# Kernel optimization log

Hardware: AMD Instinct MI355X
Metric: run time of the kernel (lower is better)

Reference implementation:

```python
import jax, jax.numpy as jnp
import numpy as np

EMB = 1024
HEADS = 16
B, N = 2, 2048

def setup_inputs() -> dict:
    key = jax.random.key(0)
    ks = jax.random.split(key, 9)
    s = 1.0 / np.sqrt(EMB)
    return {
        "x": jax.random.normal(ks[0], (B, N, EMB), dtype=jnp.float32),
        "Wq": jax.random.normal(ks[1], (EMB, EMB), dtype=jnp.float32) * s,
        "bq": jax.random.normal(ks[2], (EMB,), dtype=jnp.float32) * 0.01,
        "Wk": jax.random.normal(ks[3], (EMB, EMB), dtype=jnp.float32) * s,
        "bk": jax.random.normal(ks[4], (EMB,), dtype=jnp.float32) * 0.01,
        "Wv": jax.random.normal(ks[5], (EMB, EMB), dtype=jnp.float32) * s,
        "bv": jax.random.normal(ks[6], (EMB,), dtype=jnp.float32) * 0.01,
        "Wo": jax.random.normal(ks[7], (EMB, EMB), dtype=jnp.float32) * s,
        "bo": jax.random.normal(ks[8], (EMB,), dtype=jnp.float32) * 0.01,
    }

def _split_heads(t):
    b, n, e = t.shape
    return t.reshape(b, n, HEADS, e // HEADS).transpose(0, 2, 1, 3)  # b h n d

def reference(x, Wq, bq, Wk, bk, Wv, bv, Wo, bo):
    q = _split_heads(x @ Wq + bq)
    k = _split_heads(x @ Wk + bk)
    v = _split_heads(x @ Wv + bv)
    # NOTE: original scales by sqrt(emb_size), not sqrt(head_dim)
    scaling = jnp.asarray(EMB, x.dtype) ** 0.5
    energy = jnp.einsum('bhqd,bhkd->bhqk', q, k)
    att = jax.nn.softmax(energy / scaling, axis=-1)
    out = jnp.einsum('bhqk,bhkd->bhqd', att, v)
    out = out.transpose(0, 2, 1, 3).reshape(x.shape[0], x.shape[1], EMB)
    return out @ Wo + bo
```

## Files before the change

kernel.cpp:

```cpp
#include <hip/hip_runtime.h>
#include <hip/hip_bf16.h>

typedef __bf16 bf16_t;
typedef bf16_t bf16x8 __attribute__((ext_vector_type(8)));
typedef float f32x4 __attribute__((ext_vector_type(4)));
typedef float f32x16 __attribute__((ext_vector_type(16)));

#define EMB 1024
#define HEADS 16
#define BATCH 2
#define SEQ 2048
#define HD 64
#define TOKENS (BATCH * SEQ)

__device__ __forceinline__ void gld16(bf16_t* lds_dst, const bf16_t* g_src) {
    __builtin_amdgcn_global_load_lds(
        (const __attribute__((address_space(1))) unsigned int*)g_src,
        (__attribute__((address_space(3))) unsigned int*)lds_dst, 16, 0, 0);
}

__device__ __forceinline__ unsigned cvt_pk_bf16(float lo, float hi) {
    unsigned r;
    asm("v_cvt_pk_bf16_f32 %0, %1, %2" : "=v"(r) : "v"(lo), "v"(hi));
    return r;
}

__device__ __forceinline__ float exp2_fast(float x) {
#if __has_builtin(__builtin_amdgcn_exp2f)
    return __builtin_amdgcn_exp2f(x);
#else
    return __expf(x * 0.69314718056f);
#endif
}

__global__ __launch_bounds__(256) void convert_x(const float* __restrict__ x,
                                                 bf16_t* __restrict__ xb) {
    size_t i = ((size_t)blockIdx.x * 256 + threadIdx.x) * 16;
    f32x4 v0 = *(const f32x4*)&x[i];
    f32x4 v1 = *(const f32x4*)&x[i + 4];
    f32x4 v2 = *(const f32x4*)&x[i + 8];
    f32x4 v3 = *(const f32x4*)&x[i + 12];
    bf16x8 o0, o1;
#pragma unroll
    for (int j = 0; j < 4; ++j) {
        o0[j] = (bf16_t)v0[j]; o0[4 + j] = (bf16_t)v1[j];
        o1[j] = (bf16_t)v2[j]; o1[4 + j] = (bf16_t)v3[j];
    }
    *(bf16x8*)&xb[i] = o0;
    *(bf16x8*)&xb[i + 8] = o1;
}

__global__ __launch_bounds__(256) void prep_w(
    const float* __restrict__ W0, const float* __restrict__ W1,
    const float* __restrict__ W2, const float* __restrict__ W3,
    bf16_t* __restrict__ T0, bf16_t* __restrict__ T1,
    bf16_t* __restrict__ T2, bf16_t* __restrict__ T3) {
    __shared__ __align__(16) bf16_t T[64][72];
    int z = blockIdx.z;
    const float* src = (z == 0) ? W0 : (z == 1) ? W1 : (z == 2) ? W2 : W3;
    bf16_t* dst = (z == 0) ? T0 : (z == 1) ? T1 : (z == 2) ? T2 : T3;
    int k0 = blockIdx.y * 64, n0 = blockIdx.x * 64;
    int r = threadIdx.x >> 2, c4 = (threadIdx.x & 3) * 16;
    f32x4 v[4];
#pragma unroll
    for (int q = 0; q < 4; ++q)
        v[q] = *(const f32x4*)&src[(size_t)(k0 + r) * 1024 + n0 + c4 + q * 4];
#pragma unroll
    for (int j = 0; j < 16; ++j) T[c4 + j][r] = (bf16_t)v[j >> 2][j & 3];
    __syncthreads();
    bf16x8 o0 = *(const bf16x8*)&T[r][c4];
    bf16x8 o1 = *(const bf16x8*)&T[r][c4 + 8];
    *(bf16x8*)&dst[(size_t)(n0 + r) * 1024 + k0 + c4] = o0;
    *(bf16x8*)&dst[(size_t)(n0 + r) * 1024 + k0 + c4 + 8] = o1;
}

__global__ __launch_bounds__(256) void vtrans(const bf16_t* __restrict__ V,
                                              bf16_t* __restrict__ Vt) {
    __shared__ __align__(16) bf16_t T[64][72];
    int bh = blockIdx.y, n0 = blockIdx.x * 64;
    int r = threadIdx.x >> 2, c4 = (threadIdx.x & 3) * 16;
    const bf16_t* src = &V[((size_t)bh * SEQ + n0 + r) * HD + c4];
    bf16x8 v0 = *(const bf16x8*)&src[0];
    bf16x8 v1 = *(const bf16x8*)&src[8];
#pragma unroll
    for (int j = 0; j < 8; ++j) { T[c4 + j][r] = v0[j]; T[c4 + 8 + j][r] = v1[j]; }
    __syncthreads();
    bf16x8 o0 = *(const bf16x8*)&T[r][c4];
    bf16x8 o1 = *(const bf16x8*)&T[r][c4 + 8];
    bf16_t* dst = &Vt[((size_t)bh * HD + r) * SEQ + n0 + c4];
    *(bf16x8*)&dst[0] = o0;
    *(bf16x8*)&dst[8] = o1;
}

template <typename TO>
__global__ __launch_bounds__(256) void gemm128(
    const bf16_t* __restrict__ A,
    const bf16_t* __restrict__ Wt0, const bf16_t* __restrict__ Wt1, const bf16_t* __restrict__ Wt2,
    const float* __restrict__ b0, const float* __restrict__ b1, const float* __restrict__ b2,
    TO* __restrict__ o0, TO* __restrict__ o1, TO* __restrict__ o2,
    int md0, int md1, int md2, float sc0, float sc1, float sc2) {
    __shared__ __align__(16) bf16_t As[128 * 32];
    __shared__ __align__(16) bf16_t Bs[128 * 32];

    const int tid = threadIdx.x, w = tid >> 6, lane = tid & 63;
    const int quad = lane >> 4, c = lane & 15;
    const int wm = (w >> 1) * 64, wn = (w & 1) * 64;
    const int m0 = blockIdx.y * 128, n0 = blockIdx.x * 128;

    const int z = blockIdx.z;
    const bf16_t* W = (z == 0) ? Wt0 : (z == 1) ? Wt1 : Wt2;
    const float* bias = (z == 0) ? b0 : (z == 1) ? b1 : b2;
    TO* out = (z == 0) ? o0 : (z == 1) ? o1 : o2;
    const int mode = (z == 0) ? md0 : (z == 1) ? md1 : md2;
    const float scale = (z == 0) ? sc0 : (z == 1) ? sc1 : sc2;

    f32x4 acc[4][4];
#pragma unroll
    for (int i = 0; i < 4; ++i)
#pragma unroll
        for (int j = 0; j < 4; ++j) acc[i][j] = (f32x4){0.f, 0.f, 0.f, 0.f};

    const int srow = lane >> 2, schunk = lane & 3;
    const bf16_t* Ag = A + (size_t)m0 * 1024;
    const bf16_t* Bg = W + (size_t)n0 * 1024;

    for (int k0 = 0; k0 < 1024; k0 += 32) {
        __syncthreads();
#pragma unroll
        for (int s = 0; s < 2; ++s) {
            int rg = (w * 2 + s) * 16;
            gld16(&As[rg * 32], &Ag[(size_t)(rg + srow) * 1024 + k0 + schunk * 8]);
            gld16(&Bs[rg * 32], &Bg[(size_t)(rg + srow) * 1024 + k0 + schunk * 8]);
        }
        __syncthreads();

        bf16x8 af[4], bfv[4];
#pragma unroll
        for (int t = 0; t < 4; ++t)
            af[t] = *(const bf16x8*)&As[(wm + t * 16 + c) * 32 + quad * 8];
#pragma unroll
        for (int t = 0; t < 4; ++t)
            bfv[t] = *(const bf16x8*)&Bs[(wn + t * 16 + c) * 32 + quad * 8];
#pragma unroll
        for (int mt = 0; mt < 4; ++mt)
#pragma unroll
            for (int nt = 0; nt < 4; ++nt)
                acc[mt][nt] = __builtin_amdgcn_mfma_f32_16x16x32_bf16(
                    af[mt], bfv[nt], acc[mt][nt], 0, 0, 0);
    }

#pragma unroll
    for (int nt = 0; nt < 4; ++nt) {
        int col = n0 + wn + nt * 16 + c;
        float bv = bias[col];
#pragma unroll
        for (int mt = 0; mt < 4; ++mt)
#pragma unroll
            for (int r = 0; r < 4; ++r) {
                int row = m0 + wm + mt * 16 + quad * 4 + r;
                float v = (acc[mt][nt][r] + bv) * scale;
                size_t idx;
                if (mode == 0) {
                    idx = (size_t)row * 1024 + col;
                } else {
                    int bb = row >> 11, n = row & 2047;
                    int hh = col >> 6, d = col & 63;
                    idx = ((size_t)(bb * HEADS + hh) * SEQ + n) * HD + d;
                }
                out[idx] = (TO)v;
            }
    }
}

__global__ __launch_bounds__(256) void attn_kernel(
    const bf16_t* __restrict__ Q, const bf16_t* __restrict__ K,
    const bf16_t* __restrict__ Vt, bf16_t* __restrict__ O) {
    __shared__ __align__(16) bf16_t Qs[128 * 64];
    __shared__ __align__(16) bf16_t Ks[2][64 * 64];
    __shared__ __align__(16) bf16_t Vs[2][64 * 64];

    const int tid = threadIdx.x, w = tid >> 6, lane = tid & 63;
    const int hi = lane >> 5, lq = lane & 31;

    const int lin = blockIdx.x + (blockIdx.y << 4);
    const int xcd = lin & 7, slot = lin >> 3;
    const int bh = xcd + ((slot >> 4) << 3);
    const int q0 = (slot & 15) << 7;
    const int b = bh >> 4, h = bh & 15;

    const int srow8 = lane >> 3, sch = lane & 7;

    const bf16_t* Qg = Q + ((size_t)bh * SEQ + q0) * HD;
    const bf16_t* Kg0 = K + (size_t)bh * SEQ * HD;
    const bf16_t* Vg0 = Vt + (size_t)bh * HD * SEQ;

    int sl[2], sgK[2], sgV[2];
#pragma unroll
    for (int s = 0; s < 2; ++s) {
        int rg = (w * 2 + s) * 8;
        int row = rg + srow8;
        int g = sch ^ (row & 7);
        sl[s] = rg * 64;
        sgK[s] = row * 64 + g * 8;
        sgV[s] = row * SEQ + g * 8;
    }
    int rd[4];
#pragma unroll
    for (int dc = 0; dc < 4; ++dc)
        rd[dc] = lq * 64 + (((dc * 2 + hi) ^ (lq & 7)) * 8);

#pragma unroll
    for (int s = 0; s < 4; ++s) {
        int rg = (w * 4 + s) * 8;
        int row = rg + srow8;
        int g = sch ^ (row & 7);
        gld16(&Qs[rg * 64], &Qg[(size_t)row * 64 + g * 8]);
    }
#pragma unroll
    for (int s = 0; s < 2; ++s) {
        gld16(&Ks[0][sl[s]], &Kg0[sgK[s]]);
        gld16(&Vs[0][sl[s]], &Vg0[sgV[s]]);
    }
    __syncthreads();

    bf16x8 qf[4];
#pragma unroll
    for (int dc = 0; dc < 4; ++dc)
        qf[dc] = *(const bf16x8*)&Qs[w * 2048 + rd[dc]];

    f32x16 Oacc0, Oacc1;
#pragma unroll
    for (int r = 0; r < 16; ++r) { Oacc0[r] = 0.f; Oacc1[r] = 0.f; }
    float lp = 0.f;

    const bf16_t* KgN = Kg0 + 64 * HD;
    const bf16_t* VgN = Vg0 + 64;

#define ATTN_STEP(TT, CUR)                                                     \
    {                                                                          \
        if ((TT) + 1 < SEQ / 64) {                                             \
            _Pragma("unroll")                                                  \
            for (int s = 0; s < 2; ++s) {                                      \
                gld16(&Ks[(CUR) ^ 1][sl[s]], &KgN[sgK[s]]);                    \
                gld16(&Vs[(CUR) ^ 1][sl[s]], &VgN[sgV[s]]);                    \
            }                                                                  \
            KgN += 64 * HD; VgN += 64;                                         \
        }                                                                      \
        f32x16 St0, St1;                                                       \
        _Pragma("unroll")                                                      \
        for (int r = 0; r < 16; ++r) { St0[r] = 0.f; St1[r] = 0.f; }           \
        __builtin_amdgcn_s_setprio(1);                                         \
        _Pragma("unroll")                                                      \
        for (int dc = 0; dc < 4; ++dc) {                                       \
            bf16x8 k0 = *(const bf16x8*)&Ks[CUR][rd[dc]];                      \
            bf16x8 k1 = *(const bf16x8*)&Ks[CUR][rd[dc] + 2048];               \
            St0 = __builtin_amdgcn_mfma_f32_32x32x16_bf16(k0, qf[dc], St0, 0, 0, 0); \
            St1 = __builtin_amdgcn_mfma_f32_32x32x16_bf16(k1, qf[dc], St1, 0, 0, 0); \
        }                                                                      \
        __builtin_amdgcn_s_setprio(0);                                         \
        _Pragma("unroll")                                                      \
        for (int r = 0; r < 16; ++r) {                                         \
            St0[r] = exp2_fast(St0[r]); lp += St0[r];                          \
            St1[r] = exp2_fast(St1[r]); lp += St1[r];                          \
        }                                                                      \
        bf16x8 pf[4];                                                          \
        PACKFRAG(St0, 0, 0) PACKFRAG(St0, 1, 1)                                \
        PACKFRAG(St1, 0, 2) PACKFRAG(St1, 1, 3)                                \
        __builtin_amdgcn_s_setprio(1);                                         \
        _Pragma("unroll")                                                      \
        for (int f = 0; f < 4; ++f) {                                          \
            bf16x8 v0 = *(const bf16x8*)&Vs[CUR][rd[f]];                       \
            bf16x8 v1 = *(const bf16x8*)&Vs[CUR][rd[f] + 2048];                \
            Oacc0 = __builtin_amdgcn_mfma_f32_32x32x16_bf16(pf[f], v0, Oacc0, 0, 0, 0); \
            Oacc1 = __builtin_amdgcn_mfma_f32_32x32x16_bf16(pf[f], v1, Oacc1, 0, 0, 0); \
        }                                                                      \
        __builtin_amdgcn_s_setprio(0);                                         \
        __syncthreads();                                                       \
    }

#define PACKFRAG(SS, c2, dstIdx)                                               \
        {                                                                      \
            unsigned pa = cvt_pk_bf16(SS[8 * (c2) + 0], SS[8 * (c2) + 1]);     \
            unsigned pb = cvt_pk_bf16(SS[8 * (c2) + 4], SS[8 * (c2) + 5]);     \
            unsigned pc = cvt_pk_bf16(SS[8 * (c2) + 2], SS[8 * (c2) + 3]);     \
            unsigned pd = cvt_pk_bf16(SS[8 * (c2) + 6], SS[8 * (c2) + 7]);     \
            asm volatile("v_permlane32_swap_b32 %0, %1" : "+v"(pa), "+v"(pb)); \
            asm volatile("v_permlane32_swap_b32 %0, %1" : "+v"(pc), "+v"(pd)); \
            union { unsigned u[4]; bf16x8 v; } pu;                             \
            pu.u[0] = pa; pu.u[1] = pc; pu.u[2] = pb; pu.u[3] = pd;            \
            pf[dstIdx] = pu.v;                                                 \
        }

    for (int t = 0; t < SEQ / 64; t += 2) {
        ATTN_STEP(t, 0)
        ATTN_STEP(t + 1, 1)
    }
#undef ATTN_STEP
#undef PACKFRAG

    lp += __shfl_xor(lp, 32);
    float rl = 1.0f / lp;

#pragma unroll
    for (int r = 0; r < 16; ++r) {
        int q_loc = (r & 3) + 8 * (r >> 2) + 4 * hi;
        float rr = __shfl(rl, q_loc);
        int qrow = q0 + w * 32 + q_loc;
        size_t base = ((size_t)(b * SEQ + qrow)) * EMB + h * 64;
        O[base + lq] = (bf16_t)(Oacc0[r] * rr);
        O[base + 32 + lq] = (bf16_t)(Oacc1[r] * rr);
    }
}

extern "C" void kernel_launch(void* const* d_in, const int* in_sizes, int n_in,
                              void* d_out, int out_size, void* d_ws, size_t ws_size,
                              hipStream_t stream) {
    (void)in_sizes; (void)n_in; (void)out_size; (void)ws_size;
    const float* x  = (const float*)d_in[0];
    const float* Wq = (const float*)d_in[1];
    const float* bq = (const float*)d_in[2];
    const float* Wk = (const float*)d_in[3];
    const float* bk = (const float*)d_in[4];
    const float* Wv = (const float*)d_in[5];
    const float* bv = (const float*)d_in[6];
    const float* Wo = (const float*)d_in[7];
    const float* bo = (const float*)d_in[8];

    bf16_t* ws = (bf16_t*)d_ws;
    const size_t NELEM = (size_t)TOKENS * EMB;
    const size_t WELEM = (size_t)EMB * EMB;
    bf16_t* Qb  = ws;
    bf16_t* Kb  = ws + NELEM;
    bf16_t* Vb  = ws + 2 * NELEM;
    bf16_t* Ob  = ws + 3 * NELEM;
    bf16_t* xb  = ws + 4 * NELEM;
    bf16_t* Vtb = xb;
    bf16_t* Wt0 = ws + 5 * NELEM;
    bf16_t* Wt1 = Wt0 + WELEM;
    bf16_t* Wt2 = Wt0 + 2 * WELEM;
    bf16_t* Wt3 = Wt0 + 3 * WELEM;

    hipLaunchKernelGGL(convert_x, dim3(1024), dim3(256), 0, stream, x, xb);
    hipLaunchKernelGGL(prep_w, dim3(16, 16, 4), dim3(256), 0, stream,
                       Wq, Wk, Wv, Wo, Wt0, Wt1, Wt2, Wt3);
    hipLaunchKernelGGL((gemm128<bf16_t>), dim3(8, 32, 3), dim3(256), 0, stream,
                       xb, Wt0, Wt1, Wt2, bq, bk, bv, Qb, Kb, Vb,
                       1, 1, 1, 0.0450842204f, 1.0f, 1.0f);
    hipLaunchKernelGGL(vtrans, dim3(32, 32), dim3(256), 0, stream, Vb, Vtb);
    hipLaunchKernelGGL(attn_kernel, dim3(16, 32), dim3(256), 0, stream, Qb, Kb, Vtb, Ob);
    hipLaunchKernelGGL((gemm128<float>), dim3(8, 32, 1), dim3(256), 0, stream,
                       Ob, Wt3, Wt3, Wt3, bo, bo, bo,
                       (float*)d_out, (float*)d_out, (float*)d_out,
                       0, 0, 0, 1.0f, 1.0f, 1.0f);
}
```

Measured before the change: 214.9 us.

## Double-buffer GEMM LDS tiles, remap block indices, raise MFMA priority

```diff
diff --git a/kernel.cpp b/kernel.cpp
--- a/kernel.cpp
+++ b/kernel.cpp
@@ -99,13 +99,15 @@
     const float* __restrict__ b0, const float* __restrict__ b1, const float* __restrict__ b2,
     TO* __restrict__ o0, TO* __restrict__ o1, TO* __restrict__ o2,
     int md0, int md1, int md2, float sc0, float sc1, float sc2) {
-    __shared__ __align__(16) bf16_t As[128 * 32];
-    __shared__ __align__(16) bf16_t Bs[128 * 32];
+    __shared__ __align__(16) bf16_t As[2][128 * 32];
+    __shared__ __align__(16) bf16_t Bs[2][128 * 32];
 
     const int tid = threadIdx.x, w = tid >> 6, lane = tid & 63;
     const int quad = lane >> 4, c = lane & 15;
     const int wm = (w >> 1) * 64, wn = (w & 1) * 64;
-    const int m0 = blockIdx.y * 128, n0 = blockIdx.x * 128;
+
+    const int nx = blockIdx.y & 7, ny = blockIdx.x * 4 + (blockIdx.y >> 3);
+    const int m0 = ny * 128, n0 = nx * 128;
 
     const int z = blockIdx.z;
     const bf16_t* W = (z == 0) ? Wt0 : (z == 1) ? Wt1 : Wt2;
@@ -124,30 +126,54 @@
     const bf16_t* Ag = A + (size_t)m0 * 1024;
     const bf16_t* Bg = W + (size_t)n0 * 1024;
 
-    for (int k0 = 0; k0 < 1024; k0 += 32) {
-        __syncthreads();
-#pragma unroll
-        for (int s = 0; s < 2; ++s) {
-            int rg = (w * 2 + s) * 16;
-            gld16(&As[rg * 32], &Ag[(size_t)(rg + srow) * 1024 + k0 + schunk * 8]);
-            gld16(&Bs[rg * 32], &Bg[(size_t)(rg + srow) * 1024 + k0 + schunk * 8]);
-        }
-        __syncthreads();
-
-        bf16x8 af[4], bfv[4];
-#pragma unroll
-        for (int t = 0; t < 4; ++t)
-            af[t] = *(const bf16x8*)&As[(wm + t * 16 + c) * 32 + quad * 8];
-#pragma unroll
-        for (int t = 0; t < 4; ++t)
-            bfv[t] = *(const bf16x8*)&Bs[(wn + t * 16 + c) * 32 + quad * 8];
-#pragma unroll
-        for (int mt = 0; mt < 4; ++mt)
-#pragma unroll
-            for (int nt = 0; nt < 4; ++nt)
-                acc[mt][nt] = __builtin_amdgcn_mfma_f32_16x16x32_bf16(
-                    af[mt], bfv[nt], acc[mt][nt], 0, 0, 0);
-    }
+    int gsrc[2], ldst[2];
+#pragma unroll
+    for (int s = 0; s < 2; ++s) {
+        int rg = (w * 2 + s) * 16;
+        gsrc[s] = (rg + srow) * 1024 + schunk * 8;
+        ldst[s] = rg * 32;
+    }
+
+#pragma unroll
+    for (int s = 0; s < 2; ++s) {
+        gld16(&As[0][ldst[s]], &Ag[gsrc[s]]);
+        gld16(&Bs[0][ldst[s]], &Bg[gsrc[s]]);
+    }
+    __syncthreads();
+
+#define GEMM_STEP(TT, CUR)                                                     \
+    {                                                                          \
+        if ((TT) + 1 < 32) {                                                   \
+            int kn = ((TT) + 1) * 32;                                          \
+            _Pragma("unroll")                                                  \
+            for (int s = 0; s < 2; ++s) {                                      \
+                gld16(&As[(CUR) ^ 1][ldst[s]], &Ag[gsrc[s] + kn]);             \
+                gld16(&Bs[(CUR) ^ 1][ldst[s]], &Bg[gsrc[s] + kn]);             \
+            }                                                                  \
+        }                                                                      \
+        bf16x8 af[4], bfv[4];                                                  \
+        _Pragma("unroll")                                                      \
+        for (int t = 0; t < 4; ++t)                                            \
+            af[t] = *(const bf16x8*)&As[CUR][(wm + t * 16 + c) * 32 + quad * 8]; \
+        _Pragma("unroll")                                                      \
+        for (int t = 0; t < 4; ++t)                                            \
+            bfv[t] = *(const bf16x8*)&Bs[CUR][(wn + t * 16 + c) * 32 + quad * 8]; \
+        __builtin_amdgcn_s_setprio(1);                                         \
+        _Pragma("unroll")                                                      \
+        for (int mt = 0; mt < 4; ++mt)                                         \
+            _Pragma("unroll")                                                  \
+            for (int nt = 0; nt < 4; ++nt)                                     \
+                acc[mt][nt] = __builtin_amdgcn_mfma_f32_16x16x32_bf16(         \
+                    af[mt], bfv[nt], acc[mt][nt], 0, 0, 0);                    \
+        __builtin_amdgcn_s_setprio(0);                                         \
+        __syncthreads();                                                       \
+    }
+
+    for (int t = 0; t < 32; t += 2) {
+        GEMM_STEP(t, 0)
+        GEMM_STEP(t + 1, 1)
+    }
+#undef GEMM_STEP
 
 #pragma unroll
     for (int nt = 0; nt < 4; ++nt) {
```

After: 215.7 us. About the same (+0.4%).
